# Optimization experiments

Measured on AMD Instinct MI355X. Metric: run time of the kernel, lower is better.

## Reference

```python
import jax, jax.numpy as jnp
import numpy as np

B, T, C = 4, 2048, 1024
H = 16
D = C // H  # head_dim = 64


def setup_inputs() -> dict:
    key = jax.random.key(0)
    ks = jax.random.split(key, 9)
    s = 1.0 / np.sqrt(C)
    return {
        "x": jax.random.normal(ks[0], (B, T, C), dtype=jnp.float32),
        "Wq": jax.random.normal(ks[1], (C, C), dtype=jnp.float32) * s,
        "bq": jnp.zeros((C,), dtype=jnp.float32),
        "Wk": jax.random.normal(ks[2], (C, C), dtype=jnp.float32) * s,
        "bk": jnp.zeros((C,), dtype=jnp.float32),
        "Wv": jax.random.normal(ks[3], (C, C), dtype=jnp.float32) * s,
        "bv": jnp.zeros((C,), dtype=jnp.float32),
        "Wp": jax.random.normal(ks[4], (C, C), dtype=jnp.float32) * s,
        "bp": jnp.zeros((C,), dtype=jnp.float32),
    }


def reference(x, Wq, bq, Wk, bk, Wv, bv, Wp, bp):
    # Linear projections; reshape to [B, H, T, D]
    def split_heads(y):
        return y.reshape(B, T, H, D).transpose(0, 2, 1, 3)

    q = split_heads(x @ Wq + bq)
    k = split_heads(x @ Wk + bk)
    v = split_heads(x @ Wv + bv)

    scale = 1.0 / np.sqrt(D)
    att = jnp.einsum('bhqd,bhkd->bhqk', q, k) * scale  # [B,H,T,T]
    att = jax.nn.softmax(att, axis=-1)
    # dropout with p=0.0 is identity
    out = jnp.einsum('bhqk,bhkd->bhqd', att, v)        # [B,H,T,D]
    out = out.transpose(0, 2, 1, 3).reshape(B, T, C)
    return out @ Wp + bp
```

## Files before the change

kernel.cpp:

```cpp
#include <hip/hip_runtime.h>


#define B_ 4
#define T_ 2048
#define C_ 1024
#define H_ 16
#define D_ 64

#define QSCALE 0.18033688011112042f

typedef float  f32x4  __attribute__((ext_vector_type(4)));
typedef __bf16 bf16x8 __attribute__((ext_vector_type(8)));
typedef __bf16 bf16x4 __attribute__((ext_vector_type(4)));
typedef __bf16 bf16x2 __attribute__((ext_vector_type(2)));
typedef unsigned uint2v __attribute__((ext_vector_type(2)));

typedef const __attribute__((address_space(1))) void gv_t;
typedef __attribute__((address_space(3))) void lds_t;

__device__ __forceinline__ void async_load16(const void* g, void* l) {
  __builtin_amdgcn_global_load_lds((gv_t*)g, (lds_t*)l, 16, 0, 0);
}

__device__ __forceinline__ float fast_exp2(float x) {
#if __has_builtin(__builtin_amdgcn_exp2f)
  return __builtin_amdgcn_exp2f(x);
#else
  return exp2f(x);
#endif
}

__device__ __forceinline__ void pl16_swap(unsigned& a, unsigned& b) {
#if __has_builtin(__builtin_amdgcn_permlane16_swap)
  uint2v r = __builtin_amdgcn_permlane16_swap(a, b, false, false);
  a = r[0];
  b = r[1];
#else
  asm("v_permlane16_swap_b32 %0, %1" : "+v"(a), "+v"(b));
#endif
}

__global__ __launch_bounds__(256) void prep_kernel(
    const float* __restrict__ x, __bf16* __restrict__ xb,
    const float* __restrict__ W0, const float* __restrict__ W1,
    const float* __restrict__ W2, const float* __restrict__ W3,
    __bf16* __restrict__ wt) {
  __shared__ __align__(16) __bf16 sT[64][72];
  int l = blockIdx.x;
  int tid = threadIdx.x;
  if (l < 4096) {
    int i = (l * 256 + tid) * 8;
    float4 a = *(const float4*)(x + i);
    float4 b = *(const float4*)(x + i + 4);
    bf16x8 o;
    o[0] = (__bf16)a.x; o[1] = (__bf16)a.y; o[2] = (__bf16)a.z; o[3] = (__bf16)a.w;
    o[4] = (__bf16)b.x; o[5] = (__bf16)b.y; o[6] = (__bf16)b.z; o[7] = (__bf16)b.w;
    *(bf16x8*)(xb + i) = o;
    return;
  }
  int t = l - 4096;
  int z = t >> 8;
  int k0 = ((t >> 4) & 15) * 64;
  int n0 = (t & 15) * 64;
  const float* W = (z == 0) ? W0 : (z == 1) ? W1 : (z == 2) ? W2 : W3;
  __bf16* o = wt + (size_t)z * (C_ * C_);
#pragma unroll
  for (int i = 0; i < 4; i++) {
    int s = tid + i * 256;
    int kr = s >> 4, nc = (s & 15) * 4;
    float4 v = *(const float4*)&W[(size_t)(k0 + kr) * C_ + n0 + nc];
    bf16x4 tt;
    tt[0] = (__bf16)v.x; tt[1] = (__bf16)v.y; tt[2] = (__bf16)v.z; tt[3] = (__bf16)v.w;
    *(bf16x4*)&sT[kr][nc] = tt;
  }
  __syncthreads();
#pragma unroll
  for (int i = 0; i < 2; i++) {
    int s = tid + i * 256;
    int nr = s >> 3, kc = (s & 7) * 8;
    bf16x8 ov;
#pragma unroll
    for (int j = 0; j < 8; j++) ov[j] = sT[kc + j][nr];
    *(bf16x8*)&o[(size_t)(n0 + nr) * C_ + k0 + kc] = ov;
  }
}

template <typename OutT, int EPI, int BN>
__device__ __forceinline__ void gemm_body(
    const __bf16* __restrict__ A, const __bf16* __restrict__ Bt,
    const float* __restrict__ bias, OutT* __restrict__ C, int N, int K,
    float scale, int m0, int n0) {
  __shared__ __align__(16) __bf16 sA[128 * 32];
  __shared__ __align__(16) __bf16 sB[BN * 32];
  constexpr int NTW = BN / 32;
  constexpr int NBU = BN * 4 / 256;
  int tid = threadIdx.x, lane = tid & 63, wave = tid >> 6;
  int lr = lane & 15, quad = lane >> 4;
  int wm = (wave & 1) * 64, wn = (wave >> 1) * (BN / 2);

  const f32x4 zero = {0.f, 0.f, 0.f, 0.f};
  f32x4 acc[4][NTW];
#pragma unroll
  for (int i = 0; i < 4; i++)
#pragma unroll
    for (int j = 0; j < NTW; j++) acc[i][j] = zero;

  for (int k0 = 0; k0 < K; k0 += 32) {
    __syncthreads();
#pragma unroll
    for (int i = 0; i < 2; i++) {
      int s = tid + i * 256;
      int r = s >> 2, c8 = (s & 3) * 8;
      async_load16(A + (size_t)(m0 + r) * K + k0 + c8, &sA[s * 8]);
    }
#pragma unroll
    for (int i = 0; i < NBU; i++) {
      int s = tid + i * 256;
      int r = s >> 2, c8 = (s & 3) * 8;
      async_load16(Bt + (size_t)(n0 + r) * K + k0 + c8, &sB[s * 8]);
    }
    __syncthreads();
    bf16x8 af[4], bfr[NTW];
#pragma unroll
    for (int mt = 0; mt < 4; mt++)
      af[mt] = *(const bf16x8*)&sA[(wm + mt * 16 + lr) * 32 + quad * 8];
#pragma unroll
    for (int nt = 0; nt < NTW; nt++)
      bfr[nt] = *(const bf16x8*)&sB[(wn + nt * 16 + lr) * 32 + quad * 8];
#pragma unroll
    for (int mt = 0; mt < 4; mt++)
#pragma unroll
      for (int nt = 0; nt < NTW; nt++)
        acc[mt][nt] = __builtin_amdgcn_mfma_f32_16x16x32_bf16(
            af[mt], bfr[nt], acc[mt][nt], 0, 0, 0);
  }
  if (EPI == 0) {
#pragma unroll
    for (int mt = 0; mt < 4; mt++) {
#pragma unroll
      for (int nt = 0; nt < NTW; nt++) {
        int n = n0 + wn + nt * 16 + lr;
        float bv = bias[n];
#pragma unroll
        for (int r = 0; r < 4; r++) {
          int m = m0 + wm + mt * 16 + quad * 4 + r;
          C[(size_t)m * N + n] = (OutT)((acc[mt][nt][r] + bv) * scale);
        }
      }
    }
  } else {
    int bb = m0 >> 11;
    int mloc0 = (m0 & (T_ - 1)) + wm;
    __bf16* Ct = (__bf16*)C;
#pragma unroll
    for (int mt = 0; mt < 4; mt++) {
      int pos = ((quad & 1) << 5) | ((((quad >> 1) << 1) | (mt & 1)) << 3) |
                ((mt >> 1) << 2);
#pragma unroll
      for (int nt = 0; nt < NTW; nt++) {
        int n = n0 + wn + nt * 16 + lr;
        float bv = bias[n];
        bf16x4 ov;
#pragma unroll
        for (int r = 0; r < 4; r++) ov[r] = (__bf16)(acc[mt][nt][r] + bv);
        *(bf16x4*)&Ct[((size_t)bb * C_ + n) * T_ + mloc0 + pos] = ov;
      }
    }
  }
}

__global__ __launch_bounds__(256) void gemm_qkv_kernel(
    const __bf16* __restrict__ A, const __bf16* __restrict__ WT,
    const float* __restrict__ b0, const float* __restrict__ b1,
    const float* __restrict__ b2, __bf16* __restrict__ qkbase,
    __bf16* __restrict__ Vt) {
  int l = blockIdx.x;
  int xcd = l & 7;
  int idx = l >> 3;
  int z = idx >> 6;
  int rem = idx & 63;
  int m0 = (xcd * 8 + (rem >> 3)) * 128;
  int n0 = (rem & 7) * 128;
  if (z == 2) {
    gemm_body<__bf16, 1, 128>(A, WT + (size_t)2 * C_ * C_, b2, Vt, C_, C_,
                              1.0f, m0, n0);
  } else {
    const float* bias = (z == 0) ? b0 : b1;
    float scale = (z == 0) ? QSCALE : 1.0f;
    gemm_body<__bf16, 0, 128>(A, WT + (size_t)z * C_ * C_, bias,
                              qkbase + (size_t)z * (B_ * T_) * C_, C_, C_,
                              scale, m0, n0);
  }
}

__global__ __launch_bounds__(256) void gemm_proj_kernel(
    const __bf16* __restrict__ A, const __bf16* __restrict__ Bt,
    const float* __restrict__ bias, float* __restrict__ C) {
  int l = blockIdx.x;
  int xcd = l & 7;
  int idx = l >> 3;
  int m0 = (xcd * 8 + (idx >> 4)) * 128;
  int n0 = (idx & 15) * 64;
  gemm_body<float, 0, 64>(A, Bt, bias, C, C_, C_, 1.0f, m0, n0);
}

__global__ __launch_bounds__(256) void attn_kernel(
    const __bf16* __restrict__ Q, const __bf16* __restrict__ K,
    const __bf16* __restrict__ Vt, __bf16* __restrict__ O) {
  __shared__ __align__(16) __bf16 sK[64 * 72];
  __shared__ __align__(16) __bf16 sV[64 * 72];
  int tid = threadIdx.x, wave = tid >> 6, lane = tid & 63;
  int lr = lane & 15, quad = lane >> 4;
  int l = blockIdx.x;
  int bh = (l & 7) * 8 + ((l >> 3) & 7);
  int xbq = l >> 6;
  int b = bh >> 4, h = bh & 15;
  int qw = xbq * 256 + wave * 64;

  bf16x8 aq[4][2];
#pragma unroll
  for (int s = 0; s < 4; s++) {
    const __bf16* qp =
        Q + ((size_t)(b * T_ + qw + s * 16 + lr)) * C_ + h * D_ + quad * 8;
    aq[s][0] = *(const bf16x8*)qp;
    aq[s][1] = *(const bf16x8*)(qp + 32);
  }

  bf16x8 onesf;
#pragma unroll
  for (int j = 0; j < 8; j++) onesf[j] = (__bf16)1.0f;

  const f32x4 zero = {0.f, 0.f, 0.f, 0.f};
  f32x4 accO[4][4];
  f32x4 accL[4] = {zero, zero, zero, zero};
#pragma unroll
  for (int s = 0; s < 4; s++)
#pragma unroll
    for (int d = 0; d < 4; d++) accO[s][d] = zero;

  int srow[2], sc8[2];
#pragma unroll
  for (int i = 0; i < 2; i++) {
    int s = tid + i * 256;
    srow[i] = s >> 3;
    sc8[i] = (s & 7) * 8;
  }

  bf16x8 kreg[2], vreg[2];
#pragma unroll
  for (int i = 0; i < 2; i++) {
    kreg[i] = *(const bf16x8*)(K + ((size_t)(b * T_ + srow[i])) * C_ + h * D_ + sc8[i]);
    vreg[i] = *(const bf16x8*)(Vt + ((size_t)(bh * D_ + srow[i])) * T_ + sc8[i]);
  }

  for (int k0 = 0; k0 < T_; k0 += 64) {
    __builtin_amdgcn_sched_barrier(0);
    __builtin_amdgcn_s_barrier();
    __builtin_amdgcn_sched_barrier(0);
#pragma unroll
    for (int i = 0; i < 2; i++) {
      *(bf16x8*)&sK[srow[i] * 72 + sc8[i]] = kreg[i];
      *(bf16x8*)&sV[srow[i] * 72 + sc8[i]] = vreg[i];
    }
    __builtin_amdgcn_sched_barrier(0);
    asm volatile("s_waitcnt lgkmcnt(0)" ::: "memory");
    __builtin_amdgcn_s_barrier();
    __builtin_amdgcn_sched_barrier(0);

    if (k0 + 64 < T_) {
      int kn = k0 + 64;
#pragma unroll
      for (int i = 0; i < 2; i++) {
        kreg[i] = *(const bf16x8*)(K + ((size_t)(b * T_ + kn + srow[i])) * C_ + h * D_ + sc8[i]);
        vreg[i] = *(const bf16x8*)(Vt + ((size_t)(bh * D_ + srow[i])) * T_ + kn + sc8[i]);
      }
    }

    bf16x8 bkf[4][2];
#pragma unroll
    for (int nt = 0; nt < 4; nt++) {
      bkf[nt][0] = *(const bf16x8*)&sK[(nt * 16 + lr) * 72 + quad * 8];
      bkf[nt][1] = *(const bf16x8*)&sK[(nt * 16 + lr) * 72 + 32 + quad * 8];
    }

    bf16x8 bpA[4], bpB[4];
#pragma unroll
    for (int s = 0; s < 4; s++) {
      unsigned pw[4][2];
#pragma unroll
      for (int nt = 0; nt < 4; nt++) {
        f32x4 z = zero;
        z = __builtin_amdgcn_mfma_f32_16x16x32_bf16(bkf[nt][0], aq[s][0], z, 0, 0, 0);
        z = __builtin_amdgcn_mfma_f32_16x16x32_bf16(bkf[nt][1], aq[s][1], z, 0, 0, 0);
        union { bf16x2 h2; unsigned u; } t0, t1;
        t0.h2[0] = (__bf16)fast_exp2(z[0]);
        t0.h2[1] = (__bf16)fast_exp2(z[1]);
        t1.h2[0] = (__bf16)fast_exp2(z[2]);
        t1.h2[1] = (__bf16)fast_exp2(z[3]);
        pw[nt][0] = t0.u;
        pw[nt][1] = t1.u;
      }
      unsigned a0 = pw[0][0], b0 = pw[1][0]; pl16_swap(a0, b0);
      unsigned a1 = pw[0][1], b1 = pw[1][1]; pl16_swap(a1, b1);
      unsigned a2 = pw[2][0], b2 = pw[3][0]; pl16_swap(a2, b2);
      unsigned a3 = pw[2][1], b3 = pw[3][1]; pl16_swap(a3, b3);
      union { unsigned u[4]; bf16x8 v; } pA, pB;
      pA.u[0] = a0; pA.u[1] = a1; pA.u[2] = a2; pA.u[3] = a3;
      pB.u[0] = b0; pB.u[1] = b1; pB.u[2] = b2; pB.u[3] = b3;
      bpA[s] = pA.v;
      bpB[s] = pB.v;
      accL[s] = __builtin_amdgcn_mfma_f32_16x16x32_bf16(onesf, bpA[s], accL[s], 0, 0, 0);
      accL[s] = __builtin_amdgcn_mfma_f32_16x16x32_bf16(onesf, bpB[s], accL[s], 0, 0, 0);
    }
    __builtin_amdgcn_s_setprio(1);
#pragma unroll
    for (int dt = 0; dt < 4; dt++) {
      bf16x8 av0 = *(const bf16x8*)&sV[(dt * 16 + lr) * 72 + quad * 8];
      bf16x8 av1 = *(const bf16x8*)&sV[(dt * 16 + lr) * 72 + 32 + quad * 8];
#pragma unroll
      for (int s = 0; s < 4; s++) {
        accO[s][dt] = __builtin_amdgcn_mfma_f32_16x16x32_bf16(av0, bpA[s], accO[s][dt], 0, 0, 0);
        accO[s][dt] = __builtin_amdgcn_mfma_f32_16x16x32_bf16(av1, bpB[s], accO[s][dt], 0, 0, 0);
      }
    }
    __builtin_amdgcn_s_setprio(0);
  }

#pragma unroll
  for (int s = 0; s < 4; s++) {
    float inv = 1.0f / accL[s][0];
    __bf16* op =
        O + ((size_t)(b * T_ + qw + s * 16 + lr)) * C_ + h * D_ + quad * 4;
#pragma unroll
    for (int dt = 0; dt < 4; dt++) {
      bf16x4 ov;
#pragma unroll
      for (int r = 0; r < 4; r++) ov[r] = (__bf16)(accO[s][dt][r] * inv);
      *(bf16x4*)&op[dt * 16] = ov;
    }
  }
}

extern "C" void kernel_launch(void* const* d_in, const int* in_sizes, int n_in,
                              void* d_out, int out_size, void* d_ws, size_t ws_size,
                              hipStream_t stream) {
  const float* x  = (const float*)d_in[0];
  const float* Wq = (const float*)d_in[1];
  const float* bq = (const float*)d_in[2];
  const float* Wk = (const float*)d_in[3];
  const float* bk = (const float*)d_in[4];
  const float* Wv = (const float*)d_in[5];
  const float* bv = (const float*)d_in[6];
  const float* Wp = (const float*)d_in[7];
  const float* bp = (const float*)d_in[8];
  float* out = (float*)d_out;

  char* ws = (char*)d_ws;
  const size_t MB = 1024 * 1024;
  __bf16* xb    = (__bf16*)(ws + 0 * MB);
  __bf16* WT    = (__bf16*)(ws + 16 * MB);
  __bf16* Qb    = (__bf16*)(ws + 24 * MB);
  __bf16* Kb    = Qb + (size_t)(B_ * T_) * C_;
  __bf16* Vt    = Kb + (size_t)(B_ * T_) * C_;
  __bf16* attnb = (__bf16*)(ws + 72 * MB);
  __bf16* WpT   = WT + (size_t)3 * C_ * C_;

  prep_kernel<<<dim3(5120), dim3(256), 0, stream>>>(x, xb, Wq, Wk, Wv, Wp, WT);
  gemm_qkv_kernel<<<dim3(1536), dim3(256), 0, stream>>>(xb, WT, bq, bk, bv, Qb, Vt);
  attn_kernel<<<dim3(512), dim3(256), 0, stream>>>(Qb, Kb, Vt, attnb);
  gemm_proj_kernel<<<dim3(1024), dim3(256), 0, stream>>>(attnb, WpT, bp, out);
}
```

Before: 267.5 us.

## Double-buffer K/V shared memory tiles in attention kernel, one barrier per tile

The K and V tiles in LDS become double-buffered. Each iteration computes from one buffer while the next tile's global loads are in flight, then writes that tile into the other buffer. This cuts the per-tile synchronisation from two barriers to one, and the s_setprio priority bump around the PV MFMAs is removed. It doubles LDS use per block, which may affect occupancy.

```diff
diff --git a/kernel.cpp b/kernel.cpp
--- a/kernel.cpp
+++ b/kernel.cpp
@@ -207,8 +207,8 @@
 __global__ __launch_bounds__(256) void attn_kernel(
     const __bf16* __restrict__ Q, const __bf16* __restrict__ K,
     const __bf16* __restrict__ Vt, __bf16* __restrict__ O) {
-  __shared__ __align__(16) __bf16 sK[64 * 72];
-  __shared__ __align__(16) __bf16 sV[64 * 72];
+  __shared__ __align__(16) __bf16 sK[2][64 * 72];
+  __shared__ __align__(16) __bf16 sV[2][64 * 72];
   int tid = threadIdx.x, wave = tid >> 6, lane = tid & 63;
   int lr = lane & 15, quad = lane >> 4;
   int l = blockIdx.x;
@@ -247,40 +247,40 @@
   }
 
   bf16x8 kreg[2], vreg[2];
-#pragma unroll
-  for (int i = 0; i < 2; i++) {
-    kreg[i] = *(const bf16x8*)(K + ((size_t)(b * T_ + srow[i])) * C_ + h * D_ + sc8[i]);
-    vreg[i] = *(const bf16x8*)(Vt + ((size_t)(bh * D_ + srow[i])) * T_ + sc8[i]);
-  }
-
-  for (int k0 = 0; k0 < T_; k0 += 64) {
-    __builtin_amdgcn_sched_barrier(0);
-    __builtin_amdgcn_s_barrier();
-    __builtin_amdgcn_sched_barrier(0);
+  auto gload = [&](int k0) {
 #pragma unroll
     for (int i = 0; i < 2; i++) {
-      *(bf16x8*)&sK[srow[i] * 72 + sc8[i]] = kreg[i];
-      *(bf16x8*)&sV[srow[i] * 72 + sc8[i]] = vreg[i];
-    }
-    __builtin_amdgcn_sched_barrier(0);
-    asm volatile("s_waitcnt lgkmcnt(0)" ::: "memory");
-    __builtin_amdgcn_s_barrier();
-    __builtin_amdgcn_sched_barrier(0);
-
-    if (k0 + 64 < T_) {
-      int kn = k0 + 64;
-#pragma unroll
-      for (int i = 0; i < 2; i++) {
-        kreg[i] = *(const bf16x8*)(K + ((size_t)(b * T_ + kn + srow[i])) * C_ + h * D_ + sc8[i]);
-        vreg[i] = *(const bf16x8*)(Vt + ((size_t)(bh * D_ + srow[i])) * T_ + kn + sc8[i]);
-      }
-    }
+      kreg[i] = *(const bf16x8*)(K + ((size_t)(b * T_ + k0 + srow[i])) * C_ + h * D_ + sc8[i]);
+      vreg[i] = *(const bf16x8*)(Vt + ((size_t)(bh * D_ + srow[i])) * T_ + k0 + sc8[i]);
+    }
+  };
+  auto stage = [&](int buf) {
+#pragma unroll
+    for (int i = 0; i < 2; i++) {
+      *(bf16x8*)&sK[buf][srow[i] * 72 + sc8[i]] = kreg[i];
+      *(bf16x8*)&sV[buf][srow[i] * 72 + sc8[i]] = vreg[i];
+    }
+  };
+
+  gload(0);
+  stage(0);
+  __builtin_amdgcn_sched_barrier(0);
+  asm volatile("s_waitcnt lgkmcnt(0)" ::: "memory");
+  __builtin_amdgcn_s_barrier();
+  __builtin_amdgcn_sched_barrier(0);
+
+  const int NC = T_ / 64;
+  for (int c = 0; c < NC; c++) {
+    int buf = c & 1;
+    if (c + 1 < NC) gload((c + 1) * 64);
+    const __bf16* sKh = &sK[buf][0];
+    const __bf16* sVh = &sV[buf][0];
 
     bf16x8 bkf[4][2];
 #pragma unroll
     for (int nt = 0; nt < 4; nt++) {
-      bkf[nt][0] = *(const bf16x8*)&sK[(nt * 16 + lr) * 72 + quad * 8];
-      bkf[nt][1] = *(const bf16x8*)&sK[(nt * 16 + lr) * 72 + 32 + quad * 8];
+      bkf[nt][0] = *(const bf16x8*)&sKh[(nt * 16 + lr) * 72 + quad * 8];
+      bkf[nt][1] = *(const bf16x8*)&sKh[(nt * 16 + lr) * 72 + 32 + quad * 8];
     }
 
     bf16x8 bpA[4], bpB[4];
@@ -312,18 +312,24 @@
       accL[s] = __builtin_amdgcn_mfma_f32_16x16x32_bf16(onesf, bpA[s], accL[s], 0, 0, 0);
       accL[s] = __builtin_amdgcn_mfma_f32_16x16x32_bf16(onesf, bpB[s], accL[s], 0, 0, 0);
     }
-    __builtin_amdgcn_s_setprio(1);
 #pragma unroll
     for (int dt = 0; dt < 4; dt++) {
-      bf16x8 av0 = *(const bf16x8*)&sV[(dt * 16 + lr) * 72 + quad * 8];
-      bf16x8 av1 = *(const bf16x8*)&sV[(dt * 16 + lr) * 72 + 32 + quad * 8];
+      bf16x8 av0 = *(const bf16x8*)&sVh[(dt * 16 + lr) * 72 + quad * 8];
+      bf16x8 av1 = *(const bf16x8*)&sVh[(dt * 16 + lr) * 72 + 32 + quad * 8];
 #pragma unroll
       for (int s = 0; s < 4; s++) {
         accO[s][dt] = __builtin_amdgcn_mfma_f32_16x16x32_bf16(av0, bpA[s], accO[s][dt], 0, 0, 0);
         accO[s][dt] = __builtin_amdgcn_mfma_f32_16x16x32_bf16(av1, bpB[s], accO[s][dt], 0, 0, 0);
       }
     }
-    __builtin_amdgcn_s_setprio(0);
+
+    if (c + 1 < NC) {
+      stage(buf ^ 1);
+      __builtin_amdgcn_sched_barrier(0);
+      asm volatile("s_waitcnt lgkmcnt(0)" ::: "memory");
+      __builtin_amdgcn_s_barrier();
+      __builtin_amdgcn_sched_barrier(0);
+    }
   }
 
 #pragma unroll
```

Measured after the change: 305.2 us. +14.1%, slower.

## Split attention over key halves with fp32 partials and a combine kernel

Applied to the files above, without the earlier changes.

Attention is split along the key dimension into two halves, launching twice as many blocks. Each half writes unnormalised fp32 output and row sums to workspace, and a separate combine kernel adds them, normalises and writes bf16. This works without max rescaling only because the kernel already skips max subtraction. The aim is more parallelism and latency hiding per CU, paid for with an extra launch and roughly 128MB of fp32 partial traffic. The s_setprio hints around the PV MFMA loop are also removed.

```diff
diff --git a/kernel.cpp b/kernel.cpp
--- a/kernel.cpp
+++ b/kernel.cpp
@@ -204,16 +204,21 @@
   gemm_body<float, 0, 64>(A, Bt, bias, C, C_, C_, 1.0f, m0, n0);
 }
 
+template <int SPLIT>
 __global__ __launch_bounds__(256) void attn_kernel(
     const __bf16* __restrict__ Q, const __bf16* __restrict__ K,
-    const __bf16* __restrict__ Vt, __bf16* __restrict__ O) {
+    const __bf16* __restrict__ Vt, __bf16* __restrict__ O,
+    float* __restrict__ Opart, float* __restrict__ lpart) {
   __shared__ __align__(16) __bf16 sK[64 * 72];
   __shared__ __align__(16) __bf16 sV[64 * 72];
   int tid = threadIdx.x, wave = tid >> 6, lane = tid & 63;
   int lr = lane & 15, quad = lane >> 4;
   int l = blockIdx.x;
   int bh = (l & 7) * 8 + ((l >> 3) & 7);
-  int xbq = l >> 6;
+  int xbq = (l >> 6) & 7;
+  int half = (SPLIT == 2) ? (l >> 9) : 0;
+  int kt0 = half * (T_ / SPLIT);
+  int kt1 = kt0 + T_ / SPLIT;
   int b = bh >> 4, h = bh & 15;
   int qw = xbq * 256 + wave * 64;
 
@@ -249,11 +254,11 @@
   bf16x8 kreg[2], vreg[2];
 #pragma unroll
   for (int i = 0; i < 2; i++) {
-    kreg[i] = *(const bf16x8*)(K + ((size_t)(b * T_ + srow[i])) * C_ + h * D_ + sc8[i]);
-    vreg[i] = *(const bf16x8*)(Vt + ((size_t)(bh * D_ + srow[i])) * T_ + sc8[i]);
-  }
-
-  for (int k0 = 0; k0 < T_; k0 += 64) {
+    kreg[i] = *(const bf16x8*)(K + ((size_t)(b * T_ + kt0 + srow[i])) * C_ + h * D_ + sc8[i]);
+    vreg[i] = *(const bf16x8*)(Vt + ((size_t)(bh * D_ + srow[i])) * T_ + kt0 + sc8[i]);
+  }
+
+  for (int k0 = kt0; k0 < kt1; k0 += 64) {
     __builtin_amdgcn_sched_barrier(0);
     __builtin_amdgcn_s_barrier();
     __builtin_amdgcn_sched_barrier(0);
@@ -267,7 +272,7 @@
     __builtin_amdgcn_s_barrier();
     __builtin_amdgcn_sched_barrier(0);
 
-    if (k0 + 64 < T_) {
+    if (k0 + 64 < kt1) {
       int kn = k0 + 64;
 #pragma unroll
       for (int i = 0; i < 2; i++) {
@@ -312,7 +317,6 @@
       accL[s] = __builtin_amdgcn_mfma_f32_16x16x32_bf16(onesf, bpA[s], accL[s], 0, 0, 0);
       accL[s] = __builtin_amdgcn_mfma_f32_16x16x32_bf16(onesf, bpB[s], accL[s], 0, 0, 0);
     }
-    __builtin_amdgcn_s_setprio(1);
 #pragma unroll
     for (int dt = 0; dt < 4; dt++) {
       bf16x8 av0 = *(const bf16x8*)&sV[(dt * 16 + lr) * 72 + quad * 8];
@@ -323,22 +327,60 @@
         accO[s][dt] = __builtin_amdgcn_mfma_f32_16x16x32_bf16(av1, bpB[s], accO[s][dt], 0, 0, 0);
       }
     }
-    __builtin_amdgcn_s_setprio(0);
-  }
-
-#pragma unroll
-  for (int s = 0; s < 4; s++) {
-    float inv = 1.0f / accL[s][0];
-    __bf16* op =
-        O + ((size_t)(b * T_ + qw + s * 16 + lr)) * C_ + h * D_ + quad * 4;
-#pragma unroll
-    for (int dt = 0; dt < 4; dt++) {
-      bf16x4 ov;
-#pragma unroll
-      for (int r = 0; r < 4; r++) ov[r] = (__bf16)(accO[s][dt][r] * inv);
-      *(bf16x4*)&op[dt * 16] = ov;
-    }
-  }
+  }
+
+  if (SPLIT == 1) {
+#pragma unroll
+    for (int s = 0; s < 4; s++) {
+      float inv = 1.0f / accL[s][0];
+      __bf16* op =
+          O + ((size_t)(b * T_ + qw + s * 16 + lr)) * C_ + h * D_ + quad * 4;
+#pragma unroll
+      for (int dt = 0; dt < 4; dt++) {
+        bf16x4 ov;
+#pragma unroll
+        for (int r = 0; r < 4; r++) ov[r] = (__bf16)(accO[s][dt][r] * inv);
+        *(bf16x4*)&op[dt * 16] = ov;
+      }
+    }
+  } else {
+    float* opb = Opart + (size_t)half * (B_ * T_ * C_);
+#pragma unroll
+    for (int s = 0; s < 4; s++) {
+      float* op = opb + ((size_t)(b * T_ + qw + s * 16 + lr)) * C_ + h * D_ + quad * 4;
+#pragma unroll
+      for (int dt = 0; dt < 4; dt++) *(f32x4*)&op[dt * 16] = accO[s][dt];
+      if (quad == 0)
+        lpart[(size_t)half * (64 * T_) + (size_t)bh * T_ + qw + s * 16 + lr] =
+            accL[s][0];
+    }
+  }
+}
+
+__global__ __launch_bounds__(256) void attn_combine(
+    const float* __restrict__ Opart, const float* __restrict__ lpart,
+    __bf16* __restrict__ O) {
+  int e8 = blockIdx.x * 256 + threadIdx.x;
+  size_t e = (size_t)e8 * 8;
+  int row = e8 >> 7;
+  int c = (int)(e & 1023);
+  int bq = row >> 11;
+  int t = row & (T_ - 1);
+  int h = c >> 6;
+  float l0 = lpart[(size_t)(bq * 16 + h) * T_ + t];
+  float l1 = lpart[(size_t)(64 * T_) + (size_t)(bq * 16 + h) * T_ + t];
+  float inv = 1.0f / (l0 + l1);
+  const float* p0 = Opart + e;
+  const float* p1 = Opart + (size_t)(B_ * T_ * C_) + e;
+  f32x4 a0 = *(const f32x4*)p0, a1 = *(const f32x4*)(p0 + 4);
+  f32x4 b0 = *(const f32x4*)p1, b1 = *(const f32x4*)(p1 + 4);
+  bf16x8 o;
+#pragma unroll
+  for (int j = 0; j < 4; j++) {
+    o[j] = (__bf16)((a0[j] + b0[j]) * inv);
+    o[j + 4] = (__bf16)((a1[j] + b1[j]) * inv);
+  }
+  *(bf16x8*)(O + e) = o;
 }
 
 extern "C" void kernel_launch(void* const* d_in, const int* in_sizes, int n_in,
@@ -363,10 +405,21 @@
   __bf16* Kb    = Qb + (size_t)(B_ * T_) * C_;
   __bf16* Vt    = Kb + (size_t)(B_ * T_) * C_;
   __bf16* attnb = (__bf16*)(ws + 72 * MB);
+  float*  Opart = (float*)(ws + 88 * MB);
+  float*  lpart = (float*)(ws + 152 * MB);
   __bf16* WpT   = WT + (size_t)3 * C_ * C_;
+
+  bool split = ws_size >= 154 * MB;
 
   prep_kernel<<<dim3(5120), dim3(256), 0, stream>>>(x, xb, Wq, Wk, Wv, Wp, WT);
   gemm_qkv_kernel<<<dim3(1536), dim3(256), 0, stream>>>(xb, WT, bq, bk, bv, Qb, Vt);
-  attn_kernel<<<dim3(512), dim3(256), 0, stream>>>(Qb, Kb, Vt, attnb);
+  if (split) {
+    attn_kernel<2><<<dim3(1024), dim3(256), 0, stream>>>(Qb, Kb, Vt, attnb,
+                                                         Opart, lpart);
+    attn_combine<<<dim3(8192), dim3(256), 0, stream>>>(Opart, lpart, attnb);
+  } else {
+    attn_kernel<1><<<dim3(512), dim3(256), 0, stream>>>(Qb, Kb, Vt, attnb,
+                                                        nullptr, nullptr);
+  }
   gemm_proj_kernel<<<dim3(1024), dim3(256), 0, stream>>>(attnb, WpT, bp, out);
 }
```

Measured after the change: 301.9 us. +12.9%, slower.
